# Kernel optimization log

Measured on AMD Instinct MI355X. Metric: run time of the kernel, lower is better.

The kernel has to match this reference:

```python
import jax, jax.numpy as jnp
import numpy as np

N, E, G = 50000, 800000, 64
L, C, IN, H, OUT = 3, 4, 64, 64, 64
BN_EPS = 1e-5


def setup_inputs() -> dict:
    key = jax.random.key(0)
    ks = jax.random.split(key, 12)
    x = jax.random.normal(ks[0], (N, IN), dtype=jnp.float32)
    cluster_labels = jax.random.randint(ks[1], (N,), 0, C, dtype=jnp.int32)
    edge_index = jax.random.randint(ks[2], (2, E), 0, N, dtype=jnp.int64)
    batch = jnp.sort(jax.random.randint(ks[3], (N,), 0, G, dtype=jnp.int64))
    s1 = 1.0 / np.sqrt(H)
    # per (layer, cluster) GIN MLP params: Lin(H,H) -> BN -> ReLU -> Lin(H,H)
    W1 = jax.random.normal(ks[4], (L, C, H, H), dtype=jnp.float32) * s1
    b1 = jnp.zeros((L, C, H), dtype=jnp.float32)
    g1 = jnp.ones((L, C, H), dtype=jnp.float32)
    be1 = jnp.zeros((L, C, H), dtype=jnp.float32)
    W2 = jax.random.normal(ks[5], (L, C, H, H), dtype=jnp.float32) * s1
    b2 = jnp.zeros((L, C, H), dtype=jnp.float32)
    # pool MLP: Lin(H*L, H) -> BN -> ReLU -> Lin(H, OUT)
    Wp1 = jax.random.normal(ks[6], (H * L, H), dtype=jnp.float32) / np.sqrt(H * L)
    bp1 = jnp.zeros((H,), dtype=jnp.float32)
    gp = jnp.ones((H,), dtype=jnp.float32)
    bep = jnp.zeros((H,), dtype=jnp.float32)
    Wp2 = jax.random.normal(ks[7], (H, OUT), dtype=jnp.float32) * s1
    bp2 = jnp.zeros((OUT,), dtype=jnp.float32)
    return {"x": x, "cluster_labels": cluster_labels, "edge_index": edge_index,
            "batch": batch, "W1": W1, "b1": b1, "g1": g1, "be1": be1,
            "W2": W2, "b2": b2, "Wp1": Wp1, "bp1": bp1, "gp": gp,
            "bep": bep, "Wp2": Wp2, "bp2": bp2}


def _masked_bn(h, mf, gamma, beta):
    # BatchNorm computed only over rows where mask is set (those are the rows fed to nn)
    cnt = jnp.maximum(mf.sum(), 1.0)
    mean = (mf[:, None] * h).sum(0) / cnt
    var = (mf[:, None] * (h - mean) ** 2).sum(0) / cnt
    return (h - mean) * jax.lax.rsqrt(var + BN_EPS) * gamma + beta


def _bn(h, gamma, beta):
    mean = h.mean(0)
    var = ((h - mean) ** 2).mean(0)
    return (h - mean) * jax.lax.rsqrt(var + BN_EPS) * gamma + beta


def reference(x, cluster_labels, edge_index, batch, W1, b1, g1, be1, W2, b2,
              Wp1, bp1, gp, bep, Wp2, bp2):
    src, dst = edge_index[0], edge_index[1]
    pooled = []
    for t in range(L):
        for c in range(C):
            mask = cluster_labels == c
            mf = mask.astype(x.dtype)
            # GIN aggregation: out[i] = sum_{j -> i} x[j]
            agg = jax.ops.segment_sum(x[src], dst, num_segments=N)
            h = agg + x  # (1 + eps) * x residual with eps = 0
            h = h @ W1[t, c] + b1[t, c]
            h = jax.nn.relu(_masked_bn(h, mf, g1[t, c], be1[t, c]))
            h = h @ W2[t, c] + b2[t, c]
            x = jnp.where(mask[:, None], h, x)
        pooled.append(jax.ops.segment_sum(x, batch, num_segments=G))
    z = jnp.concatenate(pooled, axis=1)  # [G, H*L]
    z = z @ Wp1 + bp1
    z = jax.nn.relu(_bn(z, gp, bep))
    return z @ Wp2 + bp2
```

## Files before the change

### kernel.cpp

```cpp
#include <hip/hip_runtime.h>
#include <hip/hip_bf16.h>

#define NN 50000
#define EE 800000
#define GG 64
#define LL 3
#define CC 4
#define HH 64
#define BN_EPS 1e-5f
#define NSHADOW 4
#define SBLK 196
#define GIN_BLOCKS 2048
#define MM_BLOCKS 256
#define ECHUNKS 3125
#define NODE_RANGE 6250


typedef __attribute__((ext_vector_type(8))) short bf16x8;
typedef __attribute__((ext_vector_type(4))) float f32x4;

__device__ __forceinline__ float bf2f(short s) {
    return __int_as_float(((int)(unsigned short)s) << 16);
}
__device__ __forceinline__ short f2bf(float v) {
    __hip_bfloat16 hb = __float2bfloat16(v);
    return *(short*)&hb;
}


__global__ void k_deghist(const int* __restrict__ dst, int* __restrict__ deg,
                          const int* __restrict__ labels, int* __restrict__ blockcnt,
                          const float* __restrict__ x_in, __hip_bfloat16* __restrict__ xw,
                          const float* __restrict__ W1, const float* __restrict__ W2,
                          short* __restrict__ wf) {
    __shared__ int cnt[CC];
    int tid = threadIdx.x;
    for (int i = blockIdx.x * 256 + tid; i < NN * 64; i += gridDim.x * 256)
        xw[i] = __float2bfloat16(x_in[i]);
    int o = blockIdx.x * 256 + tid;
    if (o < 24 * 4096) {
        int m = o >> 12;
        int r = o & 4095;
        int colt = r >> 10;
        int fragk = (r >> 9) & 1;
        int lane = (r >> 3) & 63;
        int j = r & 7;
        int k = fragk * 32 + ((lane >> 4) << 3) + j;
        int n = colt * 16 + (lane & 15);
        const float* src = (m < 12) ? (W1 + (size_t)m * 4096) : (W2 + (size_t)(m - 12) * 4096);
        wf[o] = f2bf(src[k * 64 + n]);
    }
    bool hist = (blockIdx.x < SBLK);
    if (hist && tid < CC) cnt[tid] = 0;
    __syncthreads();
    int gid = blockIdx.x * 256 + tid;
    if (gid < EE) atomicAdd(&deg[dst[gid]], 1);
    if (hist && gid < NN) atomicAdd(&cnt[labels[gid]], 1);
    __syncthreads();
    if (hist && tid < CC) blockcnt[tid * SBLK + blockIdx.x] = cnt[tid];
}

__global__ __launch_bounds__(256) void k_scancombo(
    const int* __restrict__ deg, int* __restrict__ rowptr, int* __restrict__ dpart,
    const int* __restrict__ blockcnt, int* __restrict__ coffs, int* __restrict__ ccount) {
    __shared__ int smem[CC * 256];
    int tid = threadIdx.x;
    if (blockIdx.x < SBLK) {
        int i = blockIdx.x * 256 + tid;
        int v = (i < NN) ? deg[i] : 0;
        smem[tid] = v;
        __syncthreads();
        for (int off = 1; off < 256; off <<= 1) {
            int u = (tid >= off) ? smem[tid - off] : 0;
            __syncthreads();
            smem[tid] += u;
            __syncthreads();
        }
        if (i < NN) rowptr[i] = smem[tid] - v;
        if (tid == 255) dpart[blockIdx.x] = smem[255];
    } else {
        int own[CC];
        for (int c = 0; c < CC; c++) {
            own[c] = (tid < SBLK) ? blockcnt[c * SBLK + tid] : 0;
            smem[c * 256 + tid] = own[c];
        }
        __syncthreads();
        for (int off = 1; off < 256; off <<= 1) {
            int v[CC];
            for (int c = 0; c < CC; c++) v[c] = (tid >= off) ? smem[c * 256 + tid - off] : 0;
            __syncthreads();
            for (int c = 0; c < CC; c++) smem[c * 256 + tid] += v[c];
            __syncthreads();
        }
        if (tid < SBLK)
            for (int c = 0; c < CC; c++) coffs[c * SBLK + tid] = smem[c * 256 + tid] - own[c];
        if (tid == 0)
            for (int c = 0; c < CC; c++) ccount[c] = smem[c * 256 + 255];
    }
}

__global__ __launch_bounds__(256) void k_dscan2(int* __restrict__ dpart,
                                                int* __restrict__ dbase,
                                                int* __restrict__ rowptr) {
    __shared__ int s[256];
    int tid = threadIdx.x;
    int v = (tid < SBLK) ? dpart[tid] : 0;
    s[tid] = v;
    __syncthreads();
    for (int off = 1; off < 256; off <<= 1) {
        int u = (tid >= off) ? s[tid - off] : 0;
        __syncthreads();
        s[tid] += u;
        __syncthreads();
    }
    if (tid < SBLK) dbase[tid] = s[tid] - v;
    if (tid == 0) rowptr[NN] = EE;
}

__global__ __launch_bounds__(256) void k_cfill_dscan3(
    int* __restrict__ rowptr, const int* __restrict__ dbase, int* __restrict__ cursor,
    const int* __restrict__ labels, const int* __restrict__ coffs, int* __restrict__ clist) {
    __shared__ int pos[CC];
    int tid = threadIdx.x;
    if (tid < CC) pos[tid] = coffs[tid * SBLK + blockIdx.x];
    __syncthreads();
    int i = blockIdx.x * 256 + tid;
    if (i < NN) {
        int r = rowptr[i] + dbase[blockIdx.x];
        rowptr[i] = r;
        cursor[i] = r;
        int c = labels[i];
        int p = atomicAdd(&pos[c], 1);
        clist[c * NN + p] = i;
    }
}

__global__ void k_fill(const int* __restrict__ src, const int* __restrict__ dst,
                       int* __restrict__ cursor, int* __restrict__ adj) {
    int range = blockIdx.x / ECHUNKS;
    int e = (blockIdx.x - range * ECHUNKS) * 256 + threadIdx.x;
    if (e < EE) {
        int d = dst[e];
        int lo = range * NODE_RANGE;
        if (d >= lo && d < lo + NODE_RANGE) {
            int pos = atomicAdd(&cursor[d], 1);
            adj[pos] = src[e] << 7;
        }
    }
}

__global__ __launch_bounds__(256) void k_gather(
    const __hip_bfloat16* __restrict__ xw, const int* __restrict__ adj,
    const int* __restrict__ rowptr, const int* __restrict__ clist_c,
    const int* __restrict__ ccount_c, __hip_bfloat16* __restrict__ aggbuf,
    const int* __restrict__ batch, float* __restrict__ z, int tpool) {
    int cnt = *ccount_c;
    int lane = threadIdx.x & 63;
    int wave = threadIdx.x >> 6;
    int wid = blockIdx.x * 4 + wave;
    int nwaves = gridDim.x * 4;
    const char* xwb = (const char*)xw;
    int idx = wid;
    int node_next = (idx < cnt) ? clist_c[idx] : 0;
    for (; idx < cnt; idx += nwaves) {
        int node = node_next;
        int nidx = idx + nwaves;
        if (nidx < cnt) node_next = clist_c[nidx];
        int rb = rowptr[node], re = rowptr[node + 1];
        float a[16];
        a[0] = __bfloat162float(xw[(size_t)node * 64 + lane]);
        #pragma unroll
        for (int u = 1; u < 16; u++) a[u] = 0.f;
        int base = rb, rem = re - rb;
        while (rem > 0) {
            int take = min(rem, 64);
            int nb = adj[base + min(lane, take - 1)];
            int j = 0;
            for (; j + 16 <= take; j += 16) {
                #pragma unroll
                for (int u = 0; u < 16; u++) {
                    int o = __builtin_amdgcn_readlane(nb, j + u);
                    a[u] += __bfloat162float(((const __hip_bfloat16*)(xwb + o))[lane]);
                }
            }
            for (; j + 8 <= take; j += 8) {
                #pragma unroll
                for (int u = 0; u < 8; u++) {
                    int o = __builtin_amdgcn_readlane(nb, j + u);
                    a[u] += __bfloat162float(((const __hip_bfloat16*)(xwb + o))[lane]);
                }
            }
            for (; j < take; j++) {
                int o = __builtin_amdgcn_readlane(nb, j);
                a[0] += __bfloat162float(((const __hip_bfloat16*)(xwb + o))[lane]);
            }
            base += take; rem -= take;
        }
        float acc = (((a[0] + a[1]) + (a[2] + a[3])) + ((a[4] + a[5]) + (a[6] + a[7]))) +
                    (((a[8] + a[9]) + (a[10] + a[11])) + ((a[12] + a[13]) + (a[14] + a[15])));
        aggbuf[(size_t)idx * 64 + lane] = __float2bfloat16(acc);
    }
    if (tpool >= 0) {
        int lo = wid * 64;
        if (lo < NN) {
            int hi = min(lo + 64, NN);
            float acc = 0.f;
            int curg = batch[lo];
            for (int n = lo; n < hi; n++) {
                int g = batch[n];
                if (g != curg) {
                    atomicAdd(&z[curg * (HH * LL) + tpool * HH + lane], acc);
                    acc = 0.f;
                    curg = g;
                }
                acc += __bfloat162float(xw[(size_t)n * 64 + lane]);
            }
            atomicAdd(&z[curg * (HH * LL) + tpool * HH + lane], acc);
        }
    }
}

__global__ __launch_bounds__(256) void k_lin1(
    const __hip_bfloat16* __restrict__ aggbuf, const int* __restrict__ ccount_c,
    const short* __restrict__ wf1, const float* __restrict__ b1c,
    __hip_bfloat16* __restrict__ h1buf, float* __restrict__ bnacc) {
    int cnt = *ccount_c;
    int tiles = (cnt + 15) >> 4;
    int lane = threadIdx.x & 63;
    int wave = threadIdx.x >> 6;
    int wid = blockIdx.x * 4 + wave;
    int nwaves = gridDim.x * 4;
    int quad = lane >> 4;
    int l15 = lane & 15;

    bf16x8 wb[8];
    #pragma unroll
    for (int f = 0; f < 8; f++)
        wb[f] = *(const bf16x8*)(wf1 + f * 512 + lane * 8);
    float bcol[4];
    #pragma unroll
    for (int colt = 0; colt < 4; colt++) bcol[colt] = b1c[colt * 16 + l15];

    float sS[4] = {0.f, 0.f, 0.f, 0.f};
    float sQ[4] = {0.f, 0.f, 0.f, 0.f};

    for (int tile = wid; tile < tiles; tile += nwaves) {
        int tb = tile << 4;
        int row = tb + l15;
        const __hip_bfloat16* ar = aggbuf + (size_t)row * 64 + quad * 8;
        bf16x8 a0 = *(const bf16x8*)ar;
        bf16x8 a1 = *(const bf16x8*)(ar + 32);
        #pragma unroll
        for (int colt = 0; colt < 4; colt++) {
            f32x4 acc = {0.f, 0.f, 0.f, 0.f};
            acc = __builtin_amdgcn_mfma_f32_16x16x32_bf16(a0, wb[colt * 2 + 0], acc, 0, 0, 0);
            acc = __builtin_amdgcn_mfma_f32_16x16x32_bf16(a1, wb[colt * 2 + 1], acc, 0, 0, 0);
            #pragma unroll
            for (int r = 0; r < 4; r++) {
                int nrow = tb + quad * 4 + r;
                if (nrow < cnt) {
                    float s = acc[r] + bcol[colt];
                    __hip_bfloat16 hb = __float2bfloat16(s);
                    h1buf[(size_t)nrow * 64 + colt * 16 + l15] = hb;
                    float st = __bfloat162float(hb);
                    sS[colt] += st;
                    sQ[colt] += st * st;
                }
            }
        }
    }
    #pragma unroll
    for (int colt = 0; colt < 4; colt++) {
        sS[colt] += __shfl_xor(sS[colt], 16); sS[colt] += __shfl_xor(sS[colt], 32);
        sQ[colt] += __shfl_xor(sQ[colt], 16); sQ[colt] += __shfl_xor(sQ[colt], 32);
    }
    if (quad == 0) {
        int slot = (blockIdx.x & (NSHADOW - 1)) * 128;
        #pragma unroll
        for (int colt = 0; colt < 4; colt++) {
            atomicAdd(&bnacc[slot + colt * 16 + l15], sS[colt]);
            atomicAdd(&bnacc[slot + 64 + colt * 16 + l15], sQ[colt]);
        }
    }
}

__global__ __launch_bounds__(256) void k_cmfma(
    __hip_bfloat16* __restrict__ xw, const int* __restrict__ clist_c,
    const int* __restrict__ ccount_c, const float* __restrict__ g1c,
    const float* __restrict__ be1c, const short* __restrict__ wf2,
    const float* __restrict__ b2c, const __hip_bfloat16* __restrict__ h1buf,
    const float* __restrict__ bnacc) {
    __shared__ float lds_scale[64];
    __shared__ float lds_shift[64];
    int cnt = *ccount_c;
    int tiles = (cnt + 15) >> 4;
    int lane = threadIdx.x & 63;
    int wave = threadIdx.x >> 6;
    int wid = blockIdx.x * 4 + wave;
    int nwaves = gridDim.x * 4;
    int quad = lane >> 4;
    int l15 = lane & 15;

    if (threadIdx.x < 64) {
        float s = 0.f, q = 0.f;
        #pragma unroll
        for (int sh = 0; sh < NSHADOW; sh++) {
            s += bnacc[sh * 128 + threadIdx.x];
            q += bnacc[sh * 128 + 64 + threadIdx.x];
        }
        float fc = fmaxf((float)cnt, 1.f);
        float mean = s / fc;
        float var = q / fc - mean * mean;
        float sc = g1c[threadIdx.x] * rsqrtf(var + BN_EPS);
        lds_scale[threadIdx.x] = sc;
        lds_shift[threadIdx.x] = be1c[threadIdx.x] - mean * sc;
    }
    __syncthreads();

    bf16x8 wb[8];
    #pragma unroll
    for (int f = 0; f < 8; f++)
        wb[f] = *(const bf16x8*)(wf2 + f * 512 + lane * 8);
    float bcol[4];
    #pragma unroll
    for (int colt = 0; colt < 4; colt++) bcol[colt] = b2c[colt * 16 + l15];
    float scl0[8], sft0[8], scl1[8], sft1[8];
    #pragma unroll
    for (int j = 0; j < 8; j++) {
        int ch = quad * 8 + j;
        scl0[j] = lds_scale[ch];      sft0[j] = lds_shift[ch];
        scl1[j] = lds_scale[ch + 32]; sft1[j] = lds_shift[ch + 32];
    }

    for (int tile = wid; tile < tiles; tile += nwaves) {
        int tb = tile << 4;
        int row = tb + l15;
        const __hip_bfloat16* hr = h1buf + (size_t)row * 64 + quad * 8;
        bf16x8 h0 = *(const bf16x8*)hr;
        bf16x8 h1f = *(const bf16x8*)(hr + 32);
        bf16x8 a0, a1;
        #pragma unroll
        for (int j = 0; j < 8; j++) {
            a0[j] = f2bf(fmaxf(bf2f(h0[j]) * scl0[j] + sft0[j], 0.f));
            a1[j] = f2bf(fmaxf(bf2f(h1f[j]) * scl1[j] + sft1[j], 0.f));
        }
        #pragma unroll
        for (int colt = 0; colt < 4; colt++) {
            f32x4 acc = {0.f, 0.f, 0.f, 0.f};
            acc = __builtin_amdgcn_mfma_f32_16x16x32_bf16(a0, wb[colt * 2 + 0], acc, 0, 0, 0);
            acc = __builtin_amdgcn_mfma_f32_16x16x32_bf16(a1, wb[colt * 2 + 1], acc, 0, 0, 0);
            #pragma unroll
            for (int r = 0; r < 4; r++) {
                int nrow = tb + quad * 4 + r;
                if (nrow < cnt) {
                    int node = clist_c[nrow];
                    xw[(size_t)node * 64 + colt * 16 + l15] =
                        __float2bfloat16(acc[r] + bcol[colt]);
                }
            }
        }
    }
}

__global__ void k_pool(const __hip_bfloat16* __restrict__ xw, const int* __restrict__ batch,
                       float* __restrict__ z, int t) {
    const int CHUNK = 64;
    int lane = threadIdx.x & 63;
    int wg = (blockIdx.x * blockDim.x + threadIdx.x) >> 6;
    int lo = wg * CHUNK;
    if (lo >= NN) return;
    int hi = min(lo + CHUNK, NN);
    float acc = 0.f;
    int curg = batch[lo];
    for (int n = lo; n < hi; n++) {
        int g = batch[n];
        if (g != curg) {
            atomicAdd(&z[curg * (HH * LL) + t * HH + lane], acc);
            acc = 0.f;
            curg = g;
        }
        acc += __bfloat162float(xw[(size_t)n * 64 + lane]);
    }
    atomicAdd(&z[curg * (HH * LL) + t * HH + lane], acc);
}

__global__ __launch_bounds__(256) void k_final1(
    const float* __restrict__ z, const float* __restrict__ Wp1,
    const float* __restrict__ bp1, float* __restrict__ hbuf) {
    __shared__ float red[256];
    int g = blockIdx.x;
    int k = threadIdx.x & 63;
    int part = threadIdx.x >> 6;
    float s = 0.f;
    #pragma unroll 8
    for (int j = part * 48; j < (part + 1) * 48; j++)
        s += z[g * (HH * LL) + j] * Wp1[j * 64 + k];
    red[threadIdx.x] = s;
    __syncthreads();
    if (part == 0)
        hbuf[g * 64 + k] = red[k] + red[64 + k] + red[128 + k] + red[192 + k] + bp1[k];
}

__global__ __launch_bounds__(256) void k_final2(
    const float* __restrict__ hbuf, const float* __restrict__ gp,
    const float* __restrict__ bep, const float* __restrict__ Wp2,
    const float* __restrict__ bp2, float* __restrict__ out) {
    __shared__ float lds[64 * 64];
    __shared__ float sscale[64];
    __shared__ float sshift[64];
    int tid = threadIdx.x;
    for (int i = tid; i < 64 * 64; i += 256) lds[i] = hbuf[i];
    __syncthreads();
    if (tid < 64) {
        float s = 0.f, q = 0.f;
        for (int g = 0; g < 64; g++) { float v = lds[g * 64 + tid]; s += v; q += v * v; }
        float mean = s / 64.f;
        float var = q / 64.f - mean * mean;
        float sc = gp[tid] * rsqrtf(var + BN_EPS);
        sscale[tid] = sc;
        sshift[tid] = bep[tid] - mean * sc;
    }
    __syncthreads();
    for (int i = tid; i < 64 * 64; i += 256) {
        int k = i & 63;
        lds[i] = fmaxf(lds[i] * sscale[k] + sshift[k], 0.f);
    }
    __syncthreads();
    for (int i = tid; i < 64 * 64; i += 256) {
        int g = i >> 6, o = i & 63;
        float s = bp2[o];
        #pragma unroll 8
        for (int k = 0; k < 64; k++) s += lds[g * 64 + k] * Wp2[k * 64 + o];
        out[g * 64 + o] = s;
    }
}

extern "C" void kernel_launch(void* const* d_in, const int* in_sizes, int n_in,
                              void* d_out, int out_size, void* d_ws, size_t ws_size,
                              hipStream_t stream) {
    const float* x_in = (const float*)d_in[0];
    const int* labels = (const int*)d_in[1];
    const int* esrc = (const int*)d_in[2];
    const int* edst = esrc + EE;
    const int* batch = (const int*)d_in[3];
    const float* W1 = (const float*)d_in[4];
    const float* b1 = (const float*)d_in[5];
    const float* g1 = (const float*)d_in[6];
    const float* be1 = (const float*)d_in[7];
    const float* W2 = (const float*)d_in[8];
    const float* b2 = (const float*)d_in[9];
    const float* Wp1 = (const float*)d_in[10];
    const float* bp1 = (const float*)d_in[11];
    const float* gp = (const float*)d_in[12];
    const float* bep = (const float*)d_in[13];
    const float* Wp2 = (const float*)d_in[14];
    const float* bp2 = (const float*)d_in[15];
    float* out = (float*)d_out;

    char* p = (char*)d_ws;
    auto carve = [&](size_t bytes) -> void* {
        void* r = (void*)p;
        p += (bytes + 255) & ~(size_t)255;
        return r;
    };
    float* bnacc = (float*)carve((size_t)LL * CC * NSHADOW * 128 * 4);
    float* z     = (float*)carve((size_t)GG * HH * LL * 4);
    int*   deg   = (int*)carve((size_t)NN * 4);
    size_t zero_bytes = (size_t)(p - (char*)d_ws);
    int*   ccount  = (int*)carve(CC * 4);
    int*   blockcnt= (int*)carve((size_t)CC * SBLK * 4);
    int*   coffs   = (int*)carve((size_t)CC * SBLK * 4);
    int*   dpart   = (int*)carve((size_t)SBLK * 4);
    int*   dbase   = (int*)carve((size_t)SBLK * 4);
    __hip_bfloat16* xw     = (__hip_bfloat16*)carve((size_t)NN * 64 * 2);
    __hip_bfloat16* aggbuf = (__hip_bfloat16*)carve((size_t)NN * 64 * 2);
    __hip_bfloat16* h1buf  = (__hip_bfloat16*)carve((size_t)NN * 64 * 2);
    short* wf      = (short*)carve((size_t)24 * 4096 * 2);
    float* hbuf    = (float*)carve((size_t)GG * 64 * 4);
    int*   rowptr  = (int*)carve((size_t)(NN + 1) * 4);
    int*   cursor  = (int*)carve((size_t)NN * 4);
    int*   adj     = (int*)carve((size_t)EE * 4);
    int*   clist   = (int*)carve((size_t)CC * NN * 4);

    hipMemsetAsync(d_ws, 0, zero_bytes, stream);

    k_deghist<<<ECHUNKS, 256, 0, stream>>>(edst, deg, labels, blockcnt, x_in, xw, W1, W2, wf);
    k_scancombo<<<SBLK + 1, 256, 0, stream>>>(deg, rowptr, dpart, blockcnt, coffs, ccount);
    k_dscan2<<<1, 256, 0, stream>>>(dpart, dbase, rowptr);
    k_cfill_dscan3<<<SBLK, 256, 0, stream>>>(rowptr, dbase, cursor, labels, coffs, clist);
    k_fill<<<ECHUNKS * 8, 256, 0, stream>>>(esrc, edst, cursor, adj);

    for (int t = 0; t < LL; t++) {
        for (int c = 0; c < CC; c++) {
            int tc = t * CC + c;
            int tpool = (c == 0) ? (t - 1) : -1;
            k_gather<<<GIN_BLOCKS, 256, 0, stream>>>(
                xw, adj, rowptr, clist + c * NN, ccount + c, aggbuf, batch, z, tpool);
            k_lin1<<<MM_BLOCKS, 256, 0, stream>>>(
                aggbuf, ccount + c, wf + (size_t)tc * 4096, b1 + (size_t)tc * 64,
                h1buf, bnacc + (size_t)tc * NSHADOW * 128);
            k_cmfma<<<MM_BLOCKS, 256, 0, stream>>>(
                xw, clist + c * NN, ccount + c,
                g1 + (size_t)tc * 64, be1 + (size_t)tc * 64,
                wf + (size_t)(12 + tc) * 4096, b2 + (size_t)tc * 64,
                h1buf, bnacc + (size_t)tc * NSHADOW * 128);
        }
    }
    {
        int pool_waves = (NN + 63) / 64;
        int pool_blocks = (pool_waves * 64 + 255) / 256;
        k_pool<<<pool_blocks, 256, 0, stream>>>(xw, batch, z, LL - 1);
    }
    k_final1<<<GG, 256, 0, stream>>>(z, Wp1, bp1, hbuf);
    k_final2<<<1, 256, 0, stream>>>(hbuf, gp, bep, Wp2, bp2, out);
}
```

Measured before the change: 555.7 us.

## Fuse neighbor gather with first GIN linear layer via LDS tiles

Merges the aggregation kernel and the first MFMA linear kernel into one 1024-thread kernel. Each of 16 waves gathers one node row into an LDS tile, then 4 waves run the 16x64 MFMA and accumulate BN statistics. This removes the aggbuf global round trip and one launch per (layer, cluster). In exchange it adds block-wide barriers per tile, which couple gather latency across the 16 waves, and leaves 12 waves idle during the matmul.

```diff
diff --git a/kernel.cpp b/kernel.cpp
--- a/kernel.cpp
+++ b/kernel.cpp
@@ -10,7 +10,7 @@
 #define BN_EPS 1e-5f
 #define NSHADOW 4
 #define SBLK 196
-#define GIN_BLOCKS 2048
+#define GL_BLOCKS 512
 #define MM_BLOCKS 256
 #define ECHUNKS 3125
 #define NODE_RANGE 6250
@@ -149,58 +149,104 @@
     }
 }
 
-__global__ __launch_bounds__(256) void k_gather(
+__global__ __launch_bounds__(1024) void k_gl(
     const __hip_bfloat16* __restrict__ xw, const int* __restrict__ adj,
     const int* __restrict__ rowptr, const int* __restrict__ clist_c,
-    const int* __restrict__ ccount_c, __hip_bfloat16* __restrict__ aggbuf,
+    const int* __restrict__ ccount_c, const short* __restrict__ wf1,
+    const float* __restrict__ b1c, __hip_bfloat16* __restrict__ h1buf,
+    float* __restrict__ bnacc,
     const int* __restrict__ batch, float* __restrict__ z, int tpool) {
+    __shared__ __hip_bfloat16 lsA[16][72];
     int cnt = *ccount_c;
-    int lane = threadIdx.x & 63;
-    int wave = threadIdx.x >> 6;
-    int wid = blockIdx.x * 4 + wave;
-    int nwaves = gridDim.x * 4;
+    int tiles = (cnt + 15) >> 4;
+    int tid = threadIdx.x;
+    int lane = tid & 63;
+    int wave = tid >> 6;
+    int quad = lane >> 4;
+    int l15 = lane & 15;
     const char* xwb = (const char*)xw;
-    int idx = wid;
-    int node_next = (idx < cnt) ? clist_c[idx] : 0;
-    for (; idx < cnt; idx += nwaves) {
-        int node = node_next;
-        int nidx = idx + nwaves;
-        if (nidx < cnt) node_next = clist_c[nidx];
-        int rb = rowptr[node], re = rowptr[node + 1];
-        float a[16];
-        a[0] = __bfloat162float(xw[(size_t)node * 64 + lane]);
-        #pragma unroll
-        for (int u = 1; u < 16; u++) a[u] = 0.f;
-        int base = rb, rem = re - rb;
-        while (rem > 0) {
-            int take = min(rem, 64);
-            int nb = adj[base + min(lane, take - 1)];
-            int j = 0;
-            for (; j + 16 <= take; j += 16) {
-                #pragma unroll
-                for (int u = 0; u < 16; u++) {
-                    int o = __builtin_amdgcn_readlane(nb, j + u);
-                    a[u] += __bfloat162float(((const __hip_bfloat16*)(xwb + o))[lane]);
-                }
+
+    bf16x8 wb0, wb1;
+    float bcol = 0.f;
+    if (wave < 4) {
+        wb0 = *(const bf16x8*)(wf1 + (wave * 2 + 0) * 512 + lane * 8);
+        wb1 = *(const bf16x8*)(wf1 + (wave * 2 + 1) * 512 + lane * 8);
+        bcol = b1c[wave * 16 + l15];
+    }
+    float sS = 0.f, sQ = 0.f;
+
+    for (int tile = blockIdx.x; tile < tiles; tile += gridDim.x) {
+        int idx = (tile << 4) + wave;
+        float accv = 0.f;
+        if (idx < cnt) {
+            int node = clist_c[idx];
+            int rb = rowptr[node], re = rowptr[node + 1];
+            float a[16];
+            a[0] = __bfloat162float(xw[(size_t)node * 64 + lane]);
+            #pragma unroll
+            for (int u = 1; u < 16; u++) a[u] = 0.f;
+            int base = rb, rem = re - rb;
+            while (rem > 0) {
+                int take = min(rem, 64);
+                int nb = adj[base + min(lane, take - 1)];
+                int j = 0;
+                for (; j + 16 <= take; j += 16) {
+                    #pragma unroll
+                    for (int u = 0; u < 16; u++) {
+                        int o = __builtin_amdgcn_readlane(nb, j + u);
+                        a[u] += __bfloat162float(((const __hip_bfloat16*)(xwb + o))[lane]);
+                    }
+                }
+                for (; j + 8 <= take; j += 8) {
+                    #pragma unroll
+                    for (int u = 0; u < 8; u++) {
+                        int o = __builtin_amdgcn_readlane(nb, j + u);
+                        a[u] += __bfloat162float(((const __hip_bfloat16*)(xwb + o))[lane]);
+                    }
+                }
+                for (; j < take; j++) {
+                    int o = __builtin_amdgcn_readlane(nb, j);
+                    a[0] += __bfloat162float(((const __hip_bfloat16*)(xwb + o))[lane]);
+                }
+                base += take; rem -= take;
             }
-            for (; j + 8 <= take; j += 8) {
-                #pragma unroll
-                for (int u = 0; u < 8; u++) {
-                    int o = __builtin_amdgcn_readlane(nb, j + u);
-                    a[u] += __bfloat162float(((const __hip_bfloat16*)(xwb + o))[lane]);
+            accv = (((a[0] + a[1]) + (a[2] + a[3])) + ((a[4] + a[5]) + (a[6] + a[7]))) +
+                   (((a[8] + a[9]) + (a[10] + a[11])) + ((a[12] + a[13]) + (a[14] + a[15])));
+        }
+        lsA[wave][lane] = __float2bfloat16(accv);
+        __syncthreads();
+        if (wave < 4) {
+            bf16x8 a0 = *(const bf16x8*)&lsA[l15][quad * 8];
+            bf16x8 a1 = *(const bf16x8*)&lsA[l15][32 + quad * 8];
+            f32x4 acc = {0.f, 0.f, 0.f, 0.f};
+            acc = __builtin_amdgcn_mfma_f32_16x16x32_bf16(a0, wb0, acc, 0, 0, 0);
+            acc = __builtin_amdgcn_mfma_f32_16x16x32_bf16(a1, wb1, acc, 0, 0, 0);
+            int tb = tile << 4;
+            #pragma unroll
+            for (int r = 0; r < 4; r++) {
+                int nrow = tb + quad * 4 + r;
+                if (nrow < cnt) {
+                    float s = acc[r] + bcol;
+                    __hip_bfloat16 hb = __float2bfloat16(s);
+                    h1buf[(size_t)nrow * 64 + wave * 16 + l15] = hb;
+                    float st = __bfloat162float(hb);
+                    sS += st; sQ += st * st;
                 }
             }
-            for (; j < take; j++) {
-                int o = __builtin_amdgcn_readlane(nb, j);
-                a[0] += __bfloat162float(((const __hip_bfloat16*)(xwb + o))[lane]);
-            }
-            base += take; rem -= take;
-        }
-        float acc = (((a[0] + a[1]) + (a[2] + a[3])) + ((a[4] + a[5]) + (a[6] + a[7]))) +
-                    (((a[8] + a[9]) + (a[10] + a[11])) + ((a[12] + a[13]) + (a[14] + a[15])));
-        aggbuf[(size_t)idx * 64 + lane] = __float2bfloat16(acc);
+        }
+        __syncthreads();
+    }
+    if (wave < 4) {
+        sS += __shfl_xor(sS, 16); sS += __shfl_xor(sS, 32);
+        sQ += __shfl_xor(sQ, 16); sQ += __shfl_xor(sQ, 32);
+        if (quad == 0) {
+            int slot = (blockIdx.x & (NSHADOW - 1)) * 128;
+            atomicAdd(&bnacc[slot + wave * 16 + l15], sS);
+            atomicAdd(&bnacc[slot + 64 + wave * 16 + l15], sQ);
+        }
     }
     if (tpool >= 0) {
+        int wid = blockIdx.x * 16 + wave;
         int lo = wid * 64;
         if (lo < NN) {
             int hi = min(lo + 64, NN);
@@ -216,70 +262,6 @@
                 acc += __bfloat162float(xw[(size_t)n * 64 + lane]);
             }
             atomicAdd(&z[curg * (HH * LL) + tpool * HH + lane], acc);
-        }
-    }
-}
-
-__global__ __launch_bounds__(256) void k_lin1(
-    const __hip_bfloat16* __restrict__ aggbuf, const int* __restrict__ ccount_c,
-    const short* __restrict__ wf1, const float* __restrict__ b1c,
-    __hip_bfloat16* __restrict__ h1buf, float* __restrict__ bnacc) {
-    int cnt = *ccount_c;
-    int tiles = (cnt + 15) >> 4;
-    int lane = threadIdx.x & 63;
-    int wave = threadIdx.x >> 6;
-    int wid = blockIdx.x * 4 + wave;
-    int nwaves = gridDim.x * 4;
-    int quad = lane >> 4;
-    int l15 = lane & 15;
-
-    bf16x8 wb[8];
-    #pragma unroll
-    for (int f = 0; f < 8; f++)
-        wb[f] = *(const bf16x8*)(wf1 + f * 512 + lane * 8);
-    float bcol[4];
-    #pragma unroll
-    for (int colt = 0; colt < 4; colt++) bcol[colt] = b1c[colt * 16 + l15];
-
-    float sS[4] = {0.f, 0.f, 0.f, 0.f};
-    float sQ[4] = {0.f, 0.f, 0.f, 0.f};
-
-    for (int tile = wid; tile < tiles; tile += nwaves) {
-        int tb = tile << 4;
-        int row = tb + l15;
-        const __hip_bfloat16* ar = aggbuf + (size_t)row * 64 + quad * 8;
-        bf16x8 a0 = *(const bf16x8*)ar;
-        bf16x8 a1 = *(const bf16x8*)(ar + 32);
-        #pragma unroll
-        for (int colt = 0; colt < 4; colt++) {
-            f32x4 acc = {0.f, 0.f, 0.f, 0.f};
-            acc = __builtin_amdgcn_mfma_f32_16x16x32_bf16(a0, wb[colt * 2 + 0], acc, 0, 0, 0);
-            acc = __builtin_amdgcn_mfma_f32_16x16x32_bf16(a1, wb[colt * 2 + 1], acc, 0, 0, 0);
-            #pragma unroll
-            for (int r = 0; r < 4; r++) {
-                int nrow = tb + quad * 4 + r;
-                if (nrow < cnt) {
-                    float s = acc[r] + bcol[colt];
-                    __hip_bfloat16 hb = __float2bfloat16(s);
-                    h1buf[(size_t)nrow * 64 + colt * 16 + l15] = hb;
-                    float st = __bfloat162float(hb);
-                    sS[colt] += st;
-                    sQ[colt] += st * st;
-                }
-            }
-        }
-    }
-    #pragma unroll
-    for (int colt = 0; colt < 4; colt++) {
-        sS[colt] += __shfl_xor(sS[colt], 16); sS[colt] += __shfl_xor(sS[colt], 32);
-        sQ[colt] += __shfl_xor(sQ[colt], 16); sQ[colt] += __shfl_xor(sQ[colt], 32);
-    }
-    if (quad == 0) {
-        int slot = (blockIdx.x & (NSHADOW - 1)) * 128;
-        #pragma unroll
-        for (int colt = 0; colt < 4; colt++) {
-            atomicAdd(&bnacc[slot + colt * 16 + l15], sS[colt]);
-            atomicAdd(&bnacc[slot + 64 + colt * 16 + l15], sQ[colt]);
         }
     }
 }
@@ -472,9 +454,8 @@
     int*   coffs   = (int*)carve((size_t)CC * SBLK * 4);
     int*   dpart   = (int*)carve((size_t)SBLK * 4);
     int*   dbase   = (int*)carve((size_t)SBLK * 4);
-    __hip_bfloat16* xw     = (__hip_bfloat16*)carve((size_t)NN * 64 * 2);
-    __hip_bfloat16* aggbuf = (__hip_bfloat16*)carve((size_t)NN * 64 * 2);
-    __hip_bfloat16* h1buf  = (__hip_bfloat16*)carve((size_t)NN * 64 * 2);
+    __hip_bfloat16* xw    = (__hip_bfloat16*)carve((size_t)NN * 64 * 2);
+    __hip_bfloat16* h1buf = (__hip_bfloat16*)carve((size_t)NN * 64 * 2);
     short* wf      = (short*)carve((size_t)24 * 4096 * 2);
     float* hbuf    = (float*)carve((size_t)GG * 64 * 4);
     int*   rowptr  = (int*)carve((size_t)(NN + 1) * 4);
@@ -494,11 +475,10 @@
         for (int c = 0; c < CC; c++) {
             int tc = t * CC + c;
             int tpool = (c == 0) ? (t - 1) : -1;
-            k_gather<<<GIN_BLOCKS, 256, 0, stream>>>(
-                xw, adj, rowptr, clist + c * NN, ccount + c, aggbuf, batch, z, tpool);
-            k_lin1<<<MM_BLOCKS, 256, 0, stream>>>(
-                aggbuf, ccount + c, wf + (size_t)tc * 4096, b1 + (size_t)tc * 64,
-                h1buf, bnacc + (size_t)tc * NSHADOW * 128);
+            k_gl<<<GL_BLOCKS, 1024, 0, stream>>>(
+                xw, adj, rowptr, clist + c * NN, ccount + c,
+                wf + (size_t)tc * 4096, b1 + (size_t)tc * 64, h1buf,
+                bnacc + (size_t)tc * NSHADOW * 128, batch, z, tpool);
             k_cmfma<<<MM_BLOCKS, 256, 0, stream>>>(
                 xw, clist + c * NN, ccount + c,
                 g1 + (size_t)tc * 64, be1 + (size_t)tc * 64,
```

Result: no change. 565.1 us (+1.7%).
